# Kernel tuning notes

Hardware: AMD Instinct MI355X
Metric: run time of the kernel (lower is better)

The kernel has to match this reference:

```python
import jax, jax.numpy as jnp
import numpy as np

NUM_BINS = 256  # must be > max input value (fill_max)

def setup_inputs() -> dict:
    key = jax.random.key(0)
    inputs = jax.random.randint(key, (128, 256, 32, 32), 0, NUM_BINS, dtype=jnp.int32)
    return {"inputs": inputs}

def reference(inputs) -> jnp.ndarray:
    # Faithful to tf: reshape [B,P,S,S] -> [B, P*S*S] (tf.math.bincount flattens
    # its per-map_fn 2D input), per-batch-element histogram, max bin count.
    B = inputs.shape[0]
    flat = inputs.reshape(B, -1)  # [B, N]

    def hist_max(row):
        counts = jnp.zeros((NUM_BINS,), dtype=jnp.int32).at[row].add(1)
        return jnp.max(counts)

    out = jax.vmap(hist_max)(flat)  # [B] int32: mode frequency per batch element
    return out.astype(jnp.float32)
```

## Files before the change

### kernel.cpp

```cpp
#include <hip/hip_runtime.h>
#include <hip/hip_cooperative_groups.h>

namespace cg = cooperative_groups;


#define NUM_BINS 256
#define NREP     32
#define BPB      2
#define BLOCK    1024
#define N_PER_B  (256 * 32 * 32)
#define CHUNK    (N_PER_B / BPB)
#define NBATCH   128

__global__ __launch_bounds__(BLOCK) void
percolation_coop_kernel(const int* __restrict__ in, float* __restrict__ out,
                        int* __restrict__ part) {
    __shared__ int lh[NUM_BINS * NREP];

    for (int i = threadIdx.x; i < NUM_BINS * NREP; i += BLOCK)
        lh[i] = 0;
    __syncthreads();

    const int lane = threadIdx.x & (NREP - 1);

    const int4* p = (const int4*)(in + (size_t)blockIdx.x * CHUNK);
    const int iters = CHUNK / 4 / BLOCK;

#pragma unroll 8
    for (int i = 0; i < iters; ++i) {
        int4 v = p[(size_t)i * BLOCK + threadIdx.x];
        atomicAdd(&lh[v.x * NREP + lane], 1);
        atomicAdd(&lh[v.y * NREP + lane], 1);
        atomicAdd(&lh[v.z * NREP + lane], 1);
        atomicAdd(&lh[v.w * NREP + lane], 1);
    }
    __syncthreads();

    if (threadIdx.x < NUM_BINS) {
        int s = 0;
#pragma unroll
        for (int j = 0; j < NREP; ++j)
            s += lh[threadIdx.x * NREP + ((j + threadIdx.x) & (NREP - 1))];
        part[blockIdx.x * NUM_BINS + threadIdx.x] = s;
    }

    cg::this_grid().sync();

    if (blockIdx.x < NBATCH) {
        int v = 0;
        if (threadIdx.x < NUM_BINS) {
            const int* q = part + (size_t)blockIdx.x * BPB * NUM_BINS;
#pragma unroll
            for (int s = 0; s < BPB; ++s)
                v += q[s * NUM_BINS + threadIdx.x];
        }

#pragma unroll
        for (int off = 32; off > 0; off >>= 1)
            v = max(v, __shfl_down(v, off, 64));

        __shared__ int wmax[BLOCK / 64];
        if ((threadIdx.x & 63) == 0)
            wmax[threadIdx.x >> 6] = v;
        __syncthreads();

        if (threadIdx.x == 0) {
            int m = wmax[0];
#pragma unroll
            for (int w = 1; w < BLOCK / 64; ++w)
                m = max(m, wmax[w]);
            out[blockIdx.x] = (float)m;
        }
    }
}

extern "C" void kernel_launch(void* const* d_in, const int* in_sizes, int n_in,
                              void* d_out, int out_size, void* d_ws, size_t ws_size,
                              hipStream_t stream) {
    const int* in   = (const int*)d_in[0];
    float*     out  = (float*)d_out;
    int*       part = (int*)d_ws;

    void* args[] = { (void*)&in, (void*)&out, (void*)&part };
    hipLaunchCooperativeKernel(percolation_coop_kernel,
                               dim3(NBATCH * BPB), dim3(BLOCK),
                               args, 0, stream);
}
```

Before: 231.2 us.

## Replace cooperative grid sync with last-block-done atomic counter reduction

Drops the cooperative launch and its grid-wide barrier. Each block now publishes its partial histogram and increments a per-batch atomic counter, and the last block to arrive for a batch does the final merge and max. Blocks per batch go from 2 to 4, which gives 512 blocks for more parallelism in the histogram phase. This adds a memset launch to reset the counters and relies on acquire/release ordering through the counter.

```diff
diff --git a/kernel.cpp b/kernel.cpp
--- a/kernel.cpp
+++ b/kernel.cpp
@@ -1,21 +1,19 @@
 #include <hip/hip_runtime.h>
-#include <hip/hip_cooperative_groups.h>
-
-namespace cg = cooperative_groups;
 
 
 #define NUM_BINS 256
 #define NREP     32
-#define BPB      2
+#define BPB      4
 #define BLOCK    1024
 #define N_PER_B  (256 * 32 * 32)
 #define CHUNK    (N_PER_B / BPB)
 #define NBATCH   128
 
 __global__ __launch_bounds__(BLOCK) void
-percolation_coop_kernel(const int* __restrict__ in, float* __restrict__ out,
-                        int* __restrict__ part) {
+percolation_fused_kernel(const int* __restrict__ in, float* __restrict__ out,
+                         int* __restrict__ part, int* __restrict__ cnt) {
     __shared__ int lh[NUM_BINS * NREP];
+    __shared__ int elected;
 
     for (int i = threadIdx.x; i < NUM_BINS * NREP; i += BLOCK)
         lh[i] = 0;
@@ -36,41 +34,50 @@
     }
     __syncthreads();
 
+    const int batch = blockIdx.x >> 2;
+
     if (threadIdx.x < NUM_BINS) {
         int s = 0;
 #pragma unroll
         for (int j = 0; j < NREP; ++j)
             s += lh[threadIdx.x * NREP + ((j + threadIdx.x) & (NREP - 1))];
-        part[blockIdx.x * NUM_BINS + threadIdx.x] = s;
+        __hip_atomic_store(&part[blockIdx.x * NUM_BINS + threadIdx.x], s,
+                           __ATOMIC_RELAXED, __HIP_MEMORY_SCOPE_AGENT);
+    }
+    __syncthreads();
+
+    if (threadIdx.x == 0) {
+        int old = __hip_atomic_fetch_add(&cnt[batch], 1, __ATOMIC_ACQ_REL,
+                                         __HIP_MEMORY_SCOPE_AGENT);
+        elected = (old == BPB - 1);
+    }
+    __syncthreads();
+    if (!elected) return;
+
+    int v = 0;
+    if (threadIdx.x < NUM_BINS) {
+        const int* q = part + (size_t)batch * BPB * NUM_BINS;
+#pragma unroll
+        for (int s = 0; s < BPB; ++s)
+            v += __hip_atomic_load(&q[s * NUM_BINS + threadIdx.x],
+                                   __ATOMIC_RELAXED, __HIP_MEMORY_SCOPE_AGENT);
     }
 
-    cg::this_grid().sync();
+#pragma unroll
+    for (int off = 32; off > 0; off >>= 1)
+        v = max(v, __shfl_down(v, off, 64));
 
-    if (blockIdx.x < NBATCH) {
-        int v = 0;
-        if (threadIdx.x < NUM_BINS) {
-            const int* q = part + (size_t)blockIdx.x * BPB * NUM_BINS;
+    __shared__ int wmax[BLOCK / 64];
+    if ((threadIdx.x & 63) == 0)
+        wmax[threadIdx.x >> 6] = v;
+    __syncthreads();
+
+    if (threadIdx.x == 0) {
+        int m = wmax[0];
 #pragma unroll
-            for (int s = 0; s < BPB; ++s)
-                v += q[s * NUM_BINS + threadIdx.x];
-        }
-
-#pragma unroll
-        for (int off = 32; off > 0; off >>= 1)
-            v = max(v, __shfl_down(v, off, 64));
-
-        __shared__ int wmax[BLOCK / 64];
-        if ((threadIdx.x & 63) == 0)
-            wmax[threadIdx.x >> 6] = v;
-        __syncthreads();
-
-        if (threadIdx.x == 0) {
-            int m = wmax[0];
-#pragma unroll
-            for (int w = 1; w < BLOCK / 64; ++w)
-                m = max(m, wmax[w]);
-            out[blockIdx.x] = (float)m;
-        }
+        for (int w = 1; w < BLOCK / 64; ++w)
+            m = max(m, wmax[w]);
+        out[batch] = (float)m;
     }
 }
 
@@ -80,9 +87,8 @@
     const int* in   = (const int*)d_in[0];
     float*     out  = (float*)d_out;
     int*       part = (int*)d_ws;
+    int*       cnt  = part + NBATCH * BPB * NUM_BINS;
 
-    void* args[] = { (void*)&in, (void*)&out, (void*)&part };
-    hipLaunchCooperativeKernel(percolation_coop_kernel,
-                               dim3(NBATCH * BPB), dim3(BLOCK),
-                               args, 0, stream);
+    hipMemsetAsync(cnt, 0, NBATCH * sizeof(int), stream);
+    percolation_fused_kernel<<<NBATCH * BPB, BLOCK, 0, stream>>>(in, out, part, cnt);
 }
```

Result: faster. 207.1 us (-10.4%).
